# Performance work log

Measured on AMD Instinct MI355X. Metric: run time of the kernel, lower is better.

Reference implementation:

```python
import jax, jax.numpy as jnp
import numpy as np

NUM_HEADS = 30
EPS = 1e-5


def _fp32_layernorm(x):
    # LayerNorm over last dim, no affine, computed in fp32 (FP32LayerNorm)
    xf = x.astype(jnp.float32)
    mu = jnp.mean(xf, axis=-1, keepdims=True)
    var = jnp.mean(jnp.square(xf - mu), axis=-1, keepdims=True)
    return ((xf - mu) * jax.lax.rsqrt(var + EPS)).astype(x.dtype)


def _apply_rotary(x, cos, sin):
    # x: [B,H,S,hd]; cos/sin: [S,hd] -> broadcast via [None,None]
    half = x.shape[-1] // 2
    xr, xi = x[..., :half], x[..., half:]
    x_rot = jnp.concatenate([-xi, xr], axis=-1)
    out = x.astype(jnp.float32) * cos[None, None] + x_rot.astype(jnp.float32) * sin[None, None]
    return out.astype(x.dtype)


def setup_inputs() -> dict:
    key = jax.random.key(0)
    ks = jax.random.split(key, 12)
    B, S_img, S_txt, D = 1, 3072, 256, 1920
    hd = D // NUM_HEADS
    s = 0.02
    return {
        "hidden_states": jax.random.normal(ks[0], (B, S_img, D), jnp.float32),
        "encoder_hidden_states": jax.random.normal(ks[1], (B, S_txt, D), jnp.float32),
        "rope_cos": jax.random.normal(ks[2], (S_img, hd), jnp.float32),
        "rope_sin": jax.random.normal(ks[3], (S_img, hd), jnp.float32),
        "Wq": jax.random.normal(ks[4], (D, D), jnp.float32) * s,
        "bq": jnp.zeros((D,), jnp.float32),
        "Wk": jax.random.normal(ks[5], (D, D), jnp.float32) * s,
        "bk": jnp.zeros((D,), jnp.float32),
        "Wv": jax.random.normal(ks[6], (D, D), jnp.float32) * s,
        "bv": jnp.zeros((D,), jnp.float32),
        "Wo": jax.random.normal(ks[7], (D, D), jnp.float32) * s,
        "bo": jnp.zeros((D,), jnp.float32),
    }


def reference(hidden_states, encoder_hidden_states, rope_cos, rope_sin,
              Wq, bq, Wk, bk, Wv, bv, Wo, bo):
    T = encoder_hidden_states.shape[1]  # text_seq_length
    x = jnp.concatenate([encoder_hidden_states, hidden_states], axis=1)  # [B,S,D]
    B, S, D = x.shape
    H = NUM_HEADS
    hd = D // H

    def proj(W, b):
        return (x @ W.T + b).reshape(B, S, H, hd).transpose(0, 2, 1, 3)  # [B,H,S,hd]

    q = _fp32_layernorm(proj(Wq, bq))
    k = _fp32_layernorm(proj(Wk, bk))
    v = proj(Wv, bv)

    # partial RoPE: only the image slice (tokens after text)
    q = q.at[:, :, T:, :].set(_apply_rotary(q[:, :, T:, :], rope_cos, rope_sin))
    k = k.at[:, :, T:, :].set(_apply_rotary(k[:, :, T:, :], rope_cos, rope_sin))

    scale = 1.0 / jnp.sqrt(jnp.asarray(hd, q.dtype))
    scores = jnp.einsum("bhqd,bhkd->bhqk", q, k) * scale
    attn = jax.nn.softmax(scores, axis=-1)
    out = jnp.einsum("bhqk,bhkd->bhqd", attn, v)  # [B,H,S,hd]

    out = out.transpose(0, 2, 1, 3).reshape(B, S, D)
    out = out @ Wo.T + bo
    return (out[:, T:], out[:, :T])  # (image hidden_states, encoder_hidden_states)
```

## Files before the change

### kernel.cpp

```cpp
#include <hip/hip_runtime.h>

constexpr int S_TOT  = 3328;
constexpr int S_TXT  = 256;
constexpr int DMODEL = 1920;
constexpr int NHEAD  = 30;
constexpr int HD     = 64;

typedef _Float16 half8 __attribute__((ext_vector_type(8)));
typedef _Float16 half4v __attribute__((ext_vector_type(4)));
typedef float    f32x4 __attribute__((ext_vector_type(4)));
typedef short    bh8   __attribute__((ext_vector_type(8)));

__device__ __forceinline__ f32x4 mfma16h(half8 a, half8 b, f32x4 c) {
    return __builtin_amdgcn_mfma_f32_16x16x32_f16(a, b, c, 0, 0, 0);
}
__device__ __forceinline__ f32x4 mfma16b(bh8 a, bh8 b, f32x4 c) {
    return __builtin_amdgcn_mfma_f32_16x16x32_bf16(a, b, c, 0, 0, 0);
}
__device__ __forceinline__ void gload16(void* lds, const void* g) {
    __builtin_amdgcn_global_load_lds(
        (const __attribute__((address_space(1))) void*)g,
        (__attribute__((address_space(3))) void*)lds, 16, 0, 0);
}

__device__ __forceinline__ unsigned f2u(float x){ union{float f;unsigned u;}c; c.f=x; return c.u; }
__device__ __forceinline__ float u2f(unsigned x){ union{unsigned u;float f;}c; c.u=x; return c.f; }

__device__ __forceinline__ void split8(const float* p, bh8& hi, bh8& lo) {
    float4 f0 = *(const float4*)p;
    float4 f1 = *(const float4*)(p + 4);
    float f[8] = {f0.x, f0.y, f0.z, f0.w, f1.x, f1.y, f1.z, f1.w};
    union { bh8 v; unsigned short u[8]; } H, L;
    #pragma unroll
    for (int e = 0; e < 8; ++e) {
        unsigned ub = f2u(f[e]);
        H.u[e] = (unsigned short)(ub >> 16);
        float r = f[e] - u2f(ub & 0xFFFF0000u);
        L.u[e] = (unsigned short)(f2u(r) >> 16);
    }
    hi = H.v; lo = L.v;
}

__global__ __launch_bounds__(256) void cvt_xwv(
    const float* __restrict__ hid, const float* __restrict__ enc,
    const float* __restrict__ Wv,
    _Float16* __restrict__ xh, _Float16* __restrict__ Wvh)
{
    const int seg = blockIdx.y;
    const float* src; _Float16* dst; int n;
    switch (seg) {
        case 0:  src = enc; dst = xh;                  n = S_TXT * DMODEL;  break;
        case 1:  src = hid; dst = xh + S_TXT * DMODEL; n = 3072 * DMODEL;   break;
        default: src = Wv;  dst = Wvh;                 n = DMODEL * DMODEL; break;
    }
    for (int i = (blockIdx.x * 256 + threadIdx.x) * 4; i < n; i += gridDim.x * 256 * 4) {
        float4 v = *(const float4*)(src + i);
        half4v h = {(_Float16)v.x, (_Float16)v.y, (_Float16)v.z, (_Float16)v.w};
        *(half4v*)(dst + i) = h;
    }
}

__global__ __launch_bounds__(256) void cvt_wo(const float* __restrict__ Wo,
                                              _Float16* __restrict__ Woh)
{
    const int n = DMODEL * DMODEL;
    for (int i = (blockIdx.x * 256 + threadIdx.x) * 4; i < n; i += gridDim.x * 256 * 4) {
        float4 v = *(const float4*)(Wo + i);
        half4v h = {(_Float16)v.x, (_Float16)v.y, (_Float16)v.z, (_Float16)v.w};
        *(half4v*)(Woh + i) = h;
    }
}

__global__ __launch_bounds__(256) void gemm_v(
    const _Float16* __restrict__ xh,
    const _Float16* __restrict__ Wvh,
    const float* __restrict__ bv,
    _Float16* __restrict__ v_hT)
{
    extern __shared__ __attribute__((aligned(16))) char smem[];
    _Float16* As = (_Float16*)smem;
    _Float16* Bs = (_Float16*)(smem + 8192);

    const int tid  = threadIdx.x;
    const int wave = tid >> 6;
    const int lane = tid & 63;
    const int l16  = lane & 15;
    const int quad = lane >> 4;

    const int m0 = blockIdx.x * 128;
    const int n0 = blockIdx.y * 128;
    const int wm = (wave >> 1) * 64;
    const int wn = (wave & 1) * 64;

    const _Float16* gA = xh  + (size_t)(m0 + wave * 32 + (lane >> 2)) * DMODEL + ((lane & 3) << 3);
    const _Float16* gB = Wvh + (size_t)(n0 + wave * 32 + (lane >> 2)) * DMODEL + ((lane & 3) << 3);
    _Float16* lA = As + wave * 32 * 32;
    _Float16* lB = Bs + wave * 32 * 32;

    f32x4 acc[4][4];
    #pragma unroll
    for (int j = 0; j < 4; ++j)
        #pragma unroll
        for (int i = 0; i < 4; ++i) acc[j][i] = (f32x4){0.f, 0.f, 0.f, 0.f};

    for (int k0 = 0; k0 < DMODEL; k0 += 32) {
        __syncthreads();
        gload16(lA,        gA + k0);
        gload16(lA + 512,  gA + 16 * DMODEL + k0);
        gload16(lB,        gB + k0);
        gload16(lB + 512,  gB + 16 * DMODEL + k0);
        __syncthreads();
        half8 af[4], bf[4];
        #pragma unroll
        for (int j = 0; j < 4; ++j)
            af[j] = *(const half8*)(As + (wm + j * 16 + l16) * 32 + quad * 8);
        #pragma unroll
        for (int i = 0; i < 4; ++i)
            bf[i] = *(const half8*)(Bs + (wn + i * 16 + l16) * 32 + quad * 8);
        #pragma unroll
        for (int j = 0; j < 4; ++j)
            #pragma unroll
            for (int i = 0; i < 4; ++i)
                acc[j][i] = mfma16h(af[j], bf[i], acc[j][i]);
    }
    __syncthreads();

    const int h = (n0 + wn) / 64;
    _Float16* vt = (_Float16*)smem + wave * 64 * 72;
    #pragma unroll
    for (int j = 0; j < 4; ++j)
        #pragma unroll
        for (int r = 0; r < 4; ++r)
            #pragma unroll
            for (int i = 0; i < 4; ++i)
                vt[(i * 16 + l16) * 72 + j * 16 + quad * 4 + r] =
                    (_Float16)(acc[j][i][r] + bv[n0 + wn + i * 16 + l16]);
    __asm__ volatile("" ::: "memory");
    const int dl = lane >> 3;
    const int sl = (lane & 7) << 3;
    #pragma unroll
    for (int t = 0; t < 8; ++t) {
        const int d = t * 8 + dl;
        half8 vv = *(const half8*)(vt + d * 72 + sl);
        *(half8*)(v_hT + (size_t)(h * HD + d) * S_TOT + m0 + wm + sl) = vv;
    }
}

__global__ __launch_bounds__(256) void gemm_qk(
    const float* __restrict__ hid, const float* __restrict__ enc,
    const float* __restrict__ Wq, const float* __restrict__ Wk,
    const float* __restrict__ bq, const float* __restrict__ bk,
    const float* __restrict__ rcos, const float* __restrict__ rsin,
    _Float16* __restrict__ q_h, _Float16* __restrict__ k_h,
    _Float16* __restrict__ q_lo, _Float16* __restrict__ k_lo)
{
    extern __shared__ __attribute__((aligned(16))) char smem[];
    float* As = (float*)smem;
    float* Bs = (float*)(smem + 16384);

    const int tid  = threadIdx.x;
    const int wave = tid >> 6;
    const int lane = tid & 63;
    const int l16  = lane & 15;
    const int quad = lane >> 4;

    const int m0  = blockIdx.x * 128;
    const int n0g = blockIdx.y * 128;
    const int zz  = (n0g >= DMODEL);
    const int nloc = n0g - zz * DMODEL;
    const int wm = (wave >> 1) * 64;
    const int wn = (wave & 1) * 64;

    const float* aSrc = (m0 < S_TXT) ? (enc + (size_t)m0 * DMODEL)
                                     : (hid + (size_t)(m0 - S_TXT) * DMODEL);
    const float* bSrc = (zz ? Wk : Wq) + (size_t)nloc * DMODEL;

    const float* gA = aSrc + (size_t)(wave * 32 + (lane >> 3)) * DMODEL + ((lane & 7) << 2);
    const float* gB = bSrc + (size_t)(wave * 32 + (lane >> 3)) * DMODEL + ((lane & 7) << 2);
    float* lA = As + wave * 32 * 32;
    float* lB = Bs + wave * 32 * 32;

    f32x4 acc[4][4];
    #pragma unroll
    for (int j = 0; j < 4; ++j)
        #pragma unroll
        for (int i = 0; i < 4; ++i) acc[j][i] = (f32x4){0.f, 0.f, 0.f, 0.f};

    for (int k0 = 0; k0 < DMODEL; k0 += 32) {
        __syncthreads();
        #pragma unroll
        for (int t = 0; t < 4; ++t) {
            gload16(lA + t * 256, gA + (size_t)(t * 8) * DMODEL + k0);
            gload16(lB + t * 256, gB + (size_t)(t * 8) * DMODEL + k0);
        }
        __syncthreads();
        bh8 ah[4], al[4], bhv[4], blv[4];
        #pragma unroll
        for (int j = 0; j < 4; ++j)
            split8(As + (wm + j * 16 + l16) * 32 + quad * 8, ah[j], al[j]);
        #pragma unroll
        for (int i = 0; i < 4; ++i)
            split8(Bs + (wn + i * 16 + l16) * 32 + quad * 8, bhv[i], blv[i]);
        #pragma unroll
        for (int j = 0; j < 4; ++j)
            #pragma unroll
            for (int i = 0; i < 4; ++i) {
                acc[j][i] = mfma16b(ah[j], bhv[i], acc[j][i]);
                acc[j][i] = mfma16b(al[j], bhv[i], acc[j][i]);
                acc[j][i] = mfma16b(ah[j], blv[i], acc[j][i]);
            }
    }

    const int h = (nloc + wn) / 64;
    const float* bias = zz ? bk : bq;
    _Float16* dhi = zz ? k_h : q_h;
    _Float16* dlo = zz ? k_lo : q_lo;
    const float qscale = zz ? 1.f : 0.125f;
    const bool rope = (m0 >= S_TXT);

    #pragma unroll
    for (int j = 0; j < 4; ++j) {
        #pragma unroll
        for (int r = 0; r < 4; ++r) {
            const int s = m0 + wm + j * 16 + quad * 4 + r;
            float x[4], s1 = 0.f, s2 = 0.f;
            #pragma unroll
            for (int i = 0; i < 4; ++i) {
                x[i] = acc[j][i][r] + bias[nloc + wn + i * 16 + l16];
                s1 += x[i];
                s2 += x[i] * x[i];
            }
            #pragma unroll
            for (int off = 1; off <= 8; off <<= 1) {
                s1 += __shfl_xor(s1, off);
                s2 += __shfl_xor(s2, off);
            }
            const float mu   = s1 * (1.f / 64.f);
            const float var  = fmaxf(s2 * (1.f / 64.f) - mu * mu, 0.f);
            const float rstd = rsqrtf(var + 1e-5f);
            float xn[4];
            #pragma unroll
            for (int i = 0; i < 4; ++i) xn[i] = (x[i] - mu) * rstd;
            float o[4];
            if (rope) {
                const int pos = s - S_TXT;
                #pragma unroll
                for (int i = 0; i < 4; ++i) {
                    const int d = i * 16 + l16;
                    const float c  = rcos[(size_t)pos * HD + d];
                    const float si = rsin[(size_t)pos * HD + d];
                    const float rot = (i < 2) ? -xn[i ^ 2] : xn[i ^ 2];
                    o[i] = xn[i] * c + rot * si;
                }
            } else {
                #pragma unroll
                for (int i = 0; i < 4; ++i) o[i] = xn[i];
            }
            #pragma unroll
            for (int i = 0; i < 4; ++i) {
                const float vv = o[i] * qscale;
                const _Float16 hv = (_Float16)vv;
                const size_t idx = (size_t)(h * S_TOT + s) * HD + i * 16 + l16;
                dhi[idx] = hv;
                dlo[idx] = (_Float16)((vv - (float)hv) * 1024.f);
            }
        }
    }
}

__global__ __launch_bounds__(256, 2) void attn(
    const _Float16* __restrict__ q_h,  const _Float16* __restrict__ q_lo,
    const _Float16* __restrict__ k_h,  const _Float16* __restrict__ k_lo,
    const _Float16* __restrict__ v_hT,
    _Float16* __restrict__ aout)
{
    extern __shared__ __attribute__((aligned(16))) char smem[];
    _Float16* Ks  = (_Float16*)smem;
    _Float16* Ksl = (_Float16*)(smem + 8192);
    _Float16* Vs  = (_Float16*)(smem + 16384);
    _Float16* Pl  = (_Float16*)(smem + 24576);

    const int tid  = threadIdx.x;
    const int wave = tid >> 6;
    const int lane = tid & 63;
    const int l16  = lane & 15;
    const int quad = lane >> 4;
    const int h  = blockIdx.y;
    const int q0 = blockIdx.x * 128 + wave * 32;

    const _Float16* qbase  = q_h  + (size_t)(h * S_TOT + q0) * HD;
    const _Float16* qlbase = q_lo + (size_t)(h * S_TOT + q0) * HD;
    half8 aq0[2], aq1[2], aql0[2], aql1[2];
    #pragma unroll
    for (int j = 0; j < 2; ++j) {
        aq0[j]  = *(const half8*)(qbase  + (j * 16 + l16) * HD + quad * 8);
        aq1[j]  = *(const half8*)(qbase  + (j * 16 + l16) * HD + 32 + quad * 8);
        aql0[j] = *(const half8*)(qlbase + (j * 16 + l16) * HD + quad * 8);
        aql1[j] = *(const half8*)(qlbase + (j * 16 + l16) * HD + 32 + quad * 8);
    }

    const _Float16* kbase  = k_h  + (size_t)h * S_TOT * HD;
    const _Float16* klbase = k_lo + (size_t)h * S_TOT * HD;
    const _Float16* vbase  = v_hT + (size_t)h * HD * S_TOT;

    const int srow = lane >> 3;
    const int schk = ((lane & 7) ^ srow) << 3;
    const _Float16* gK0  = kbase  + (size_t)(wave * 16 + srow) * HD + schk;
    const _Float16* gKl0 = klbase + (size_t)(wave * 16 + srow) * HD + schk;
    const _Float16* gV0  = vbase  + (size_t)(wave * 16 + srow) * S_TOT + schk;
    _Float16* lK0  = Ks  + (wave * 16) * 64;
    _Float16* lKl0 = Ksl + (wave * 16) * 64;
    _Float16* lV0  = Vs  + (wave * 16) * 64;

    const int c0 = (quad ^ (l16 & 7)) << 3;
    const int c1 = c0 ^ 32;

    f32x4 o[2][4];
    float m_i[2][4], l_i[2][4];
    #pragma unroll
    for (int j = 0; j < 2; ++j)
        #pragma unroll
        for (int i = 0; i < 4; ++i) {
            o[j][i] = (f32x4){0.f, 0.f, 0.f, 0.f};
            m_i[j][i] = -1e30f; l_i[j][i] = 0.f;
        }

    for (int kv0 = 0; kv0 < S_TOT; kv0 += 64) {
        __syncthreads();
        gload16(lK0,        gK0  + (size_t)kv0 * HD);
        gload16(lK0 + 512,  gK0  + (size_t)(kv0 + 8) * HD);
        gload16(lKl0,       gKl0 + (size_t)kv0 * HD);
        gload16(lKl0 + 512, gKl0 + (size_t)(kv0 + 8) * HD);
        gload16(lV0,        gV0 + kv0);
        gload16(lV0 + 512,  gV0 + kv0 + 8 * S_TOT);
        __syncthreads();
        f32x4 sc[2][4];
        #pragma unroll
        for (int i = 0; i < 4; ++i) {
            const int rb = (i * 16 + l16) * 64;
            half8 b0 = *(const half8*)(Ks  + rb + c0);
            half8 b1 = *(const half8*)(Ks  + rb + c1);
            half8 d0 = *(const half8*)(Ksl + rb + c0);
            half8 d1 = *(const half8*)(Ksl + rb + c1);
            #pragma unroll
            for (int j = 0; j < 2; ++j) {
                f32x4 s  = (f32x4){0.f, 0.f, 0.f, 0.f};
                f32x4 s2 = (f32x4){0.f, 0.f, 0.f, 0.f};
                s  = mfma16h(aq0[j],  b0, s);   s  = mfma16h(aq1[j],  b1, s);
                s2 = mfma16h(aql0[j], b0, s2);  s2 = mfma16h(aql1[j], b1, s2);
                s2 = mfma16h(aq0[j],  d0, s2);  s2 = mfma16h(aq1[j],  d1, s2);
                sc[j][i] = s + s2 * 0.0009765625f;
            }
        }
        #pragma unroll
        for (int j = 0; j < 2; ++j)
            #pragma unroll
            for (int r = 0; r < 4; ++r) {
                float mx = fmaxf(fmaxf(sc[j][0][r], sc[j][1][r]),
                                 fmaxf(sc[j][2][r], sc[j][3][r]));
                mx = fmaxf(mx, __shfl_xor(mx, 1));
                mx = fmaxf(mx, __shfl_xor(mx, 2));
                mx = fmaxf(mx, __shfl_xor(mx, 4));
                mx = fmaxf(mx, __shfl_xor(mx, 8));
                const float mnew  = fmaxf(m_i[j][r], mx);
                const float alpha = __expf(m_i[j][r] - mnew);
                m_i[j][r] = mnew;
                float rs = 0.f;
                #pragma unroll
                for (int i = 0; i < 4; ++i) {
                    float p = __expf(sc[j][i][r] - mnew);
                    rs += p;
                    Pl[(wave * 32 + j * 16 + quad * 4 + r) * 72 + i * 16 + l16] = (_Float16)p;
                }
                l_i[j][r] = l_i[j][r] * alpha + rs;
                #pragma unroll
                for (int i = 0; i < 4; ++i) o[j][i][r] *= alpha;
            }
        __asm__ volatile("" ::: "memory");
        half8 ap0[2], ap1[2];
        #pragma unroll
        for (int j = 0; j < 2; ++j) {
            ap0[j] = *(const half8*)(Pl + (wave * 32 + j * 16 + l16) * 72 + quad * 8);
            ap1[j] = *(const half8*)(Pl + (wave * 32 + j * 16 + l16) * 72 + 32 + quad * 8);
        }
        #pragma unroll
        for (int i = 0; i < 4; ++i) {
            const int rb = (i * 16 + l16) * 64;
            half8 vb0 = *(const half8*)(Vs + rb + c0);
            half8 vb1 = *(const half8*)(Vs + rb + c1);
            #pragma unroll
            for (int j = 0; j < 2; ++j) {
                o[j][i] = mfma16h(ap0[j], vb0, o[j][i]);
                o[j][i] = mfma16h(ap1[j], vb1, o[j][i]);
            }
        }
    }
    #pragma unroll
    for (int j = 0; j < 2; ++j)
        #pragma unroll
        for (int r = 0; r < 4; ++r) {
            float l = l_i[j][r];
            l += __shfl_xor(l, 1);
            l += __shfl_xor(l, 2);
            l += __shfl_xor(l, 4);
            l += __shfl_xor(l, 8);
            const float inv = 1.f / l;
            const int srow2 = q0 + j * 16 + quad * 4 + r;
            #pragma unroll
            for (int i = 0; i < 4; ++i)
                aout[(size_t)srow2 * DMODEL + h * HD + i * 16 + l16] =
                    (_Float16)(o[j][i][r] * inv);
        }
}

__global__ __launch_bounds__(256) void gemm_out(
    const _Float16* __restrict__ A,
    const _Float16* __restrict__ Woh,
    const float* __restrict__ bo,
    float* __restrict__ out)
{
    extern __shared__ __attribute__((aligned(16))) char smem[];
    _Float16* As = (_Float16*)smem;
    _Float16* Bs = (_Float16*)(smem + 8192);

    const int tid  = threadIdx.x;
    const int wave = tid >> 6;
    const int lane = tid & 63;
    const int l16  = lane & 15;
    const int quad = lane >> 4;

    const int m0 = blockIdx.x * 128;
    const int n0 = blockIdx.y * 128;
    const int wm = (wave >> 1) * 64;
    const int wn = (wave & 1) * 64;

    const _Float16* gA = A   + (size_t)(m0 + wave * 32 + (lane >> 2)) * DMODEL + ((lane & 3) << 3);
    const _Float16* gB = Woh + (size_t)(n0 + wave * 32 + (lane >> 2)) * DMODEL + ((lane & 3) << 3);
    _Float16* lA = As + wave * 32 * 32;
    _Float16* lB = Bs + wave * 32 * 32;

    f32x4 acc[4][4];
    #pragma unroll
    for (int j = 0; j < 4; ++j)
        #pragma unroll
        for (int i = 0; i < 4; ++i) acc[j][i] = (f32x4){0.f, 0.f, 0.f, 0.f};

    for (int k0 = 0; k0 < DMODEL; k0 += 32) {
        __syncthreads();
        gload16(lA,        gA + k0);
        gload16(lA + 512,  gA + 16 * DMODEL + k0);
        gload16(lB,        gB + k0);
        gload16(lB + 512,  gB + 16 * DMODEL + k0);
        __syncthreads();
        half8 af[4], bf[4];
        #pragma unroll
        for (int j = 0; j < 4; ++j)
            af[j] = *(const half8*)(As + (wm + j * 16 + l16) * 32 + quad * 8);
        #pragma unroll
        for (int i = 0; i < 4; ++i)
            bf[i] = *(const half8*)(Bs + (wn + i * 16 + l16) * 32 + quad * 8);
        #pragma unroll
        for (int j = 0; j < 4; ++j)
            #pragma unroll
            for (int i = 0; i < 4; ++i)
                acc[j][i] = mfma16h(af[j], bf[i], acc[j][i]);
    }
    #pragma unroll
    for (int j = 0; j < 4; ++j) {
        #pragma unroll
        for (int i = 0; i < 4; ++i) {
            const int n = n0 + wn + i * 16 + l16;
            const float bb = bo[n];
            #pragma unroll
            for (int r = 0; r < 4; ++r) {
                const int m = m0 + wm + j * 16 + quad * 4 + r;
                const int orow = (m >= S_TXT) ? (m - S_TXT) : (m + 3072);
                out[(size_t)orow * DMODEL + n] = acc[j][i][r] + bb;
            }
        }
    }
}

extern "C" void kernel_launch(void* const* d_in, const int* in_sizes, int n_in,
                              void* d_out, int out_size, void* d_ws, size_t ws_size,
                              hipStream_t stream) {
    const float* hid  = (const float*)d_in[0];
    const float* enc  = (const float*)d_in[1];
    const float* rcos = (const float*)d_in[2];
    const float* rsin = (const float*)d_in[3];
    const float* Wq   = (const float*)d_in[4];
    const float* bq   = (const float*)d_in[5];
    const float* Wk   = (const float*)d_in[6];
    const float* bk   = (const float*)d_in[7];
    const float* Wv   = (const float*)d_in[8];
    const float* bv   = (const float*)d_in[9];
    const float* Wo   = (const float*)d_in[10];
    const float* bo   = (const float*)d_in[11];

    char* ws = (char*)d_ws;
    _Float16* xh   = (_Float16*)(ws + 0);
    _Float16* aout = (_Float16*)(ws + 0);
    _Float16* q_h  = (_Float16*)(ws + 12779520);
    _Float16* Woh  = (_Float16*)(ws + 12779520);
    _Float16* k_h  = (_Float16*)(ws + 25559040);
    _Float16* v_hT = (_Float16*)(ws + 38338560);
    _Float16* Wvh  = (_Float16*)d_out;
    _Float16* q_lo = (_Float16*)d_out;
    _Float16* k_lo = (_Float16*)((char*)d_out + 12779520);

    cvt_xwv<<<dim3(128, 3), 256, 0, stream>>>(hid, enc, Wv, xh, Wvh);
    gemm_v<<<dim3(26, 15), 256, 36864, stream>>>(xh, Wvh, bv, v_hT);
    gemm_qk<<<dim3(26, 30), 256, 32768, stream>>>(
        hid, enc, Wq, Wk, bq, bk, rcos, rsin, q_h, k_h, q_lo, k_lo);
    attn<<<dim3(26, NHEAD), 256, 43008, stream>>>(q_h, q_lo, k_h, k_lo, v_hT, aout);
    cvt_wo<<<dim3(128), 256, 0, stream>>>(Wo, Woh);
    gemm_out<<<dim3(26, 15), 256, 16384, stream>>>(aout, Woh, bo, (float*)d_out);
}
```

Measured before the change: 854.6 us.

## Double-buffer K/V tiles in attention kernel with async LDS prefetch

The attention kernel now keeps two LDS buffers for the K, K-low and V tiles. It issues the global-to-LDS loads for the next tile before computing on the current one, using a partial vmcnt wait in place of the old two full syncthreads per tile. The goal is to hide global load latency behind the MFMA work. In exchange, LDS use per block grows to about 66 KB, which may cut how many blocks fit per CU, and the raw s_barrier calls depend on the waitcnt ordering being correct.

Measured after the change: 850.8 us. About the same (-0.4%).

```diff
diff --git a/kernel.cpp b/kernel.cpp
--- a/kernel.cpp
+++ b/kernel.cpp
@@ -275,10 +275,10 @@
     _Float16* __restrict__ aout)
 {
     extern __shared__ __attribute__((aligned(16))) char smem[];
-    _Float16* Ks  = (_Float16*)smem;
-    _Float16* Ksl = (_Float16*)(smem + 8192);
-    _Float16* Vs  = (_Float16*)(smem + 16384);
-    _Float16* Pl  = (_Float16*)(smem + 24576);
+    _Float16* KsB  = (_Float16*)smem;
+    _Float16* KslB = (_Float16*)(smem + 16384);
+    _Float16* VsB  = (_Float16*)(smem + 32768);
+    _Float16* Pl   = (_Float16*)(smem + 49152);
 
     const int tid  = threadIdx.x;
     const int wave = tid >> 6;
@@ -305,12 +305,9 @@
 
     const int srow = lane >> 3;
     const int schk = ((lane & 7) ^ srow) << 3;
-    const _Float16* gK0  = kbase  + (size_t)(wave * 16 + srow) * HD + schk;
-    const _Float16* gKl0 = klbase + (size_t)(wave * 16 + srow) * HD + schk;
-    const _Float16* gV0  = vbase  + (size_t)(wave * 16 + srow) * S_TOT + schk;
-    _Float16* lK0  = Ks  + (wave * 16) * 64;
-    _Float16* lKl0 = Ksl + (wave * 16) * 64;
-    _Float16* lV0  = Vs  + (wave * 16) * 64;
+    const _Float16* gK  = kbase  + (size_t)(wave * 16 + srow) * HD + schk;
+    const _Float16* gKl = klbase + (size_t)(wave * 16 + srow) * HD + schk;
+    const _Float16* gV  = vbase  + (size_t)(wave * 16 + srow) * S_TOT + schk;
 
     const int c0 = (quad ^ (l16 & 7)) << 3;
     const int c1 = c0 ^ 32;
@@ -325,15 +322,34 @@
             m_i[j][i] = -1e30f; l_i[j][i] = 0.f;
         }
 
-    for (int kv0 = 0; kv0 < S_TOT; kv0 += 64) {
-        __syncthreads();
-        gload16(lK0,        gK0  + (size_t)kv0 * HD);
-        gload16(lK0 + 512,  gK0  + (size_t)(kv0 + 8) * HD);
-        gload16(lKl0,       gKl0 + (size_t)kv0 * HD);
-        gload16(lKl0 + 512, gKl0 + (size_t)(kv0 + 8) * HD);
-        gload16(lV0,        gV0 + kv0);
-        gload16(lV0 + 512,  gV0 + kv0 + 8 * S_TOT);
-        __syncthreads();
+    constexpr int NT = S_TOT / 64;
+
+    auto stage = [&](int kv0, int p) {
+        _Float16* lK  = KsB  + p * 4096 + wave * 1024;
+        _Float16* lKl = KslB + p * 4096 + wave * 1024;
+        _Float16* lV  = VsB  + p * 4096 + wave * 1024;
+        gload16(lK,        gK  + (size_t)kv0 * HD);
+        gload16(lK + 512,  gK  + (size_t)(kv0 + 8) * HD);
+        gload16(lKl,       gKl + (size_t)kv0 * HD);
+        gload16(lKl + 512, gKl + (size_t)(kv0 + 8) * HD);
+        gload16(lV,        gV + kv0);
+        gload16(lV + 512,  gV + kv0 + 8 * S_TOT);
+    };
+
+    stage(0, 0);
+    for (int t = 0; t < NT; ++t) {
+        const int cur = t & 1;
+        if (t + 1 < NT) {
+            stage((t + 1) * 64, cur ^ 1);
+            asm volatile("s_waitcnt vmcnt(6)" ::: "memory");
+        } else {
+            asm volatile("s_waitcnt vmcnt(0)" ::: "memory");
+        }
+        __builtin_amdgcn_s_barrier();
+        const _Float16* Ks  = KsB  + cur * 4096;
+        const _Float16* Ksl = KslB + cur * 4096;
+        const _Float16* Vs  = VsB  + cur * 4096;
+
         f32x4 sc[2][4];
         #pragma unroll
         for (int i = 0; i < 4; ++i) {
@@ -394,6 +410,7 @@
                 o[j][i] = mfma16h(ap1[j], vb1, o[j][i]);
             }
         }
+        __builtin_amdgcn_s_barrier();
     }
     #pragma unroll
     for (int j = 0; j < 2; ++j)
@@ -508,11 +525,18 @@
     _Float16* q_lo = (_Float16*)d_out;
     _Float16* k_lo = (_Float16*)((char*)d_out + 12779520);
 
+    static bool attn_attr_set = false;
+    if (!attn_attr_set) {
+        (void)hipFuncSetAttribute(reinterpret_cast<const void*>(&attn),
+                                  hipFuncAttributeMaxDynamicSharedMemorySize, 67584);
+        attn_attr_set = true;
+    }
+
     cvt_xwv<<<dim3(128, 3), 256, 0, stream>>>(hid, enc, Wv, xh, Wvh);
     gemm_v<<<dim3(26, 15), 256, 36864, stream>>>(xh, Wvh, bv, v_hT);
     gemm_qk<<<dim3(26, 30), 256, 32768, stream>>>(
         hid, enc, Wq, Wk, bq, bk, rcos, rsin, q_h, k_h, q_lo, k_lo);
-    attn<<<dim3(26, NHEAD), 256, 43008, stream>>>(q_h, q_lo, k_h, k_lo, v_hT, aout);
+    attn<<<dim3(26, NHEAD), 256, 67584, stream>>>(q_h, q_lo, k_h, k_lo, v_hT, aout);
     cvt_wo<<<dim3(128), 256, 0, stream>>>(Wo, Woh);
     gemm_out<<<dim3(26, 15), 256, 16384, stream>>>(aout, Woh, bo, (float*)d_out);
 }
```
